# Optimization experiments

Hardware: AMD Instinct MI355X
Metric: run time of the kernel (lower is better)

The kernel has to match this reference:

```python
import jax, jax.numpy as jnp
import numpy as np

N, D_IN, D, C, TOPK = 8192, 1024, 512, 2, 6
SCALE = D ** -0.5
LN_EPS = 1e-5


def setup_inputs() -> dict:
    key = jax.random.key(0)
    ks = jax.random.split(key, 20)
    s = 0.02
    p = {
        'x': jax.random.normal(ks[0], (N, D_IN), jnp.float32),
        'fc1_w': jax.random.normal(ks[1], (D_IN, D)) * s,
        'fc1_b': jnp.zeros((D,)),
        'wh_w': jax.random.normal(ks[2], (D, D)) * s,
        'wh_b': jnp.zeros((D,)),
        'wt_w': jax.random.normal(ks[3], (D, D)) * s,
        'wt_b': jnp.zeros((D,)),
        'lin1_w': jax.random.normal(ks[4], (D, D)) * s,
        'lin1_b': jnp.zeros((D,)),
        'lin2_w': jax.random.normal(ks[5], (D, D)) * s,
        'lin2_b': jnp.zeros((D,)),
        'att1_w': jax.random.normal(ks[6], (D, D // 2)) * s,
        'att1_b': jnp.zeros((D // 2,)),
        'att2_w': jax.random.normal(ks[7], (D // 2, 1)) * s,
        'att2_b': jnp.zeros((1,)),
        'ln_g': jnp.ones((D,)),
        'ln_b': jnp.zeros((D,)),
        'fc_w': jax.random.normal(ks[8], (D, C)) * s,
        'fc_b': jnp.zeros((C,)),
    }
    return p


def reference(x, fc1_w, fc1_b, wh_w, wh_b, wt_w, wt_b, lin1_w, lin1_b,
              lin2_w, lin2_b, att1_w, att1_b, att2_w, att2_b, ln_g, ln_b,
              fc_w, fc_b):
    # _fc1: Linear + ReLU (dropout = eval identity)
    h = jax.nn.relu(x @ fc1_w + fc1_b)                      # [N, D]
    h = (h + h.mean(axis=0, keepdims=True)) * 0.5
    e_h = h @ wh_w + wh_b                                   # [N, D]
    e_t = h @ wt_w + wt_b                                   # [N, D]
    # dense N x N attention logits, then top-k neighbors
    logits = (e_h * SCALE) @ e_t.T                          # [N, N]
    tw, ti = jax.lax.top_k(logits, TOPK)                    # [N, K]
    Nb_h = e_t[ti]                                          # [N, K, D] gather
    p = jax.nn.softmax(tw, axis=-1)                         # [N, K]
    # eh_r = p * Nb_h + (1 - p) * e_h  (the matmul in torch is a broadcast)
    eh_r = p[..., None] * Nb_h + (1.0 - p)[..., None] * e_h[:, None, :]
    gate = jnp.tanh(e_h[:, None, :] + eh_r)                 # [N, K, D]
    ka = jnp.einsum('nkd,nkd->nk', Nb_h, gate)              # [N, K]
    kp = jax.nn.softmax(ka, axis=-1)                        # [N, K]
    e_Nh = jnp.einsum('nk,nkd->nd', kp, Nb_h)               # [N, D]
    sum_e = jax.nn.leaky_relu((e_h + e_Nh) @ lin1_w + lin1_b)
    bi_e = jax.nn.leaky_relu((e_h * e_Nh) @ lin2_w + lin2_b)
    emb = sum_e + bi_e                                      # [N, D]
    # GlobalAttention readout over all N nodes (batch=None -> one graph)
    att = jax.nn.leaky_relu(emb @ att1_w + att1_b) @ att2_w + att2_b  # [N,1]
    a = jax.nn.softmax(att, axis=0)                         # [N, 1]
    pooled = jnp.sum(a * emb, axis=0, keepdims=True)        # [1, D]
    # LayerNorm
    mu = pooled.mean(axis=-1, keepdims=True)
    var = pooled.var(axis=-1, keepdims=True)
    ln = (pooled - mu) * jax.lax.rsqrt(var + LN_EPS) * ln_g + ln_b
    out = ln @ fc_w + fc_b                                  # [1, C]
    Y_prob = jax.nn.softmax(out, axis=-1)
    Y_hat = jnp.argmax(out, axis=-1, keepdims=True)
    return out, Y_prob, Y_hat
```

## Files before the change

### kernel.cpp

```cpp
#include <hip/hip_runtime.h>
#include <hip/hip_bf16.h>
#include <cstdint>
#include <math.h>

typedef unsigned short u16;
typedef unsigned int u32;
typedef __bf16 bh;
typedef bh bh8 __attribute__((ext_vector_type(8)));
typedef float f32x4 __attribute__((ext_vector_type(4)));

#define SCALE_F 0.04419417382415922f

__device__ __forceinline__ float bf2f(u16 u) {
    union { float f; unsigned int i; } v; v.i = ((unsigned int)u) << 16; return v.f;
}
__device__ __forceinline__ u16 f2bf(float f) {
    __hip_bfloat16 h = __float2bfloat16(f);
    return __builtin_bit_cast(u16, h);
}
__device__ __forceinline__ bh8 ld8_f32(const float* p) {
    float4 f0 = *(const float4*)p;
    float4 f1 = *(const float4*)(p + 4);
    bh8 r;
    r[0] = (bh)f0.x; r[1] = (bh)f0.y; r[2] = (bh)f0.z; r[3] = (bh)f0.w;
    r[4] = (bh)f1.x; r[5] = (bh)f1.y; r[6] = (bh)f1.z; r[7] = (bh)f1.w;
    return r;
}

__device__ __forceinline__ u32 ordf(float f) {
    u32 u = __float_as_uint(f);
    return u ^ ((u32)((int)u >> 31) | 0x80000000u);
}
__device__ __forceinline__ float unordf(u32 s) {
    u32 u = (s & 0x80000000u) ? (s ^ 0x80000000u) : ~s;
    return __uint_as_float(u);
}
__device__ __forceinline__ u32 pack_vi(float v, int inv_idx) {
    return (ordf(v) & 0xFFFFFF00u) | (u32)inv_idx;
}
__device__ __forceinline__ float unpack_v(u32 p) {
    return unordf(p & 0xFFFFFF00u);
}

__device__ __forceinline__ void gl_lds16(const u16* g, u16* l) {
    __builtin_amdgcn_global_load_lds(
        (const __attribute__((address_space(1))) void*)g,
        (__attribute__((address_space(3))) void*)l, 16, 0, 0);
}

__global__ void transpose_cvt(const float* s0, u16* d0, const float* s1, u16* d1,
                              const float* s2, u16* d2, const float* s3, u16* d3,
                              const float* s4, u16* d4, const float* s5, u16* d5,
                              const float* xs, u16* xd) {
    int b = blockIdx.x;
    if (b >= 1664) {
        int t = threadIdx.y * 32 + threadIdx.x;
        size_t i = ((size_t)(b - 1664) * 256 + t) * 8;
        *(bh8*)(xd + i) = ld8_f32(xs + i);
        return;
    }
    __shared__ float tsh[32][33];
    const float* src; u16* dst; int R, C, tt;
    if      (b < 512)  { src = s0; dst = d0; R = 1024; C = 512; tt = b; }
    else if (b < 768)  { src = s1; dst = d1; R = 512;  C = 512; tt = b - 512; }
    else if (b < 1024) { src = s2; dst = d2; R = 512;  C = 512; tt = b - 768; }
    else if (b < 1280) { src = s3; dst = d3; R = 512;  C = 512; tt = b - 1024; }
    else if (b < 1536) { src = s4; dst = d4; R = 512;  C = 512; tt = b - 1280; }
    else               { src = s5; dst = d5; R = 512;  C = 256; tt = b - 1536; }
    int ntx = C >> 5;
    int bx = (tt % ntx) * 32, by = (tt / ntx) * 32;
    int x = threadIdx.x, y = threadIdx.y;
    for (int i = 0; i < 32; i += 8)
        tsh[y + i][x] = src[(size_t)(by + y + i) * C + bx + x];
    __syncthreads();
    for (int i = 0; i < 32; i += 8)
        dst[(size_t)(bx + y + i) * R + by + x] = f2bf(tsh[x][y + i]);
}

template<int KT, int NF>
__device__ __forceinline__ void kloop64(const u16* __restrict__ Ag, const u16* __restrict__ Bg,
                                        u16* Alds, u16* Blds, f32x4 (&acc)[2][NF]) {
    const int tid = threadIdx.x;
    const int wave = tid >> 6, lane = tid & 63;
    const int lr = lane & 15, quad = lane >> 4;
    const int wm = (wave & 1) * 32, wn = (wave >> 1) * (NF * 16);
    const int r = tid >> 2;
    const int g8 = (((tid & 3) ^ ((tid >> 3) & 3))) * 8;
    const int kbr8 = (quad ^ ((lr >> 1) & 3)) * 8;
    const u16* ga  = Ag + (size_t)r * KT + g8;
    const u16* gb0 = Bg + (size_t)r * KT + g8;
    const u16* gb1 = gb0 + (size_t)64 * KT;
    u16* la = Alds + wave * 512;
    u16* lb = Blds + wave * 512;
    #pragma unroll
    for (int k0 = 0; k0 < KT; k0 += 32) {
        __syncthreads();
        gl_lds16(ga + k0, la);
        gl_lds16(gb0 + k0, lb);
        if (NF == 4) gl_lds16(gb1 + k0, lb + 2048);
        __syncthreads();
        bh8 af[2], bf_[NF];
        #pragma unroll
        for (int i = 0; i < 2; i++)
            af[i] = *(const bh8*)&Alds[(wm + i * 16 + lr) * 32 + kbr8];
        #pragma unroll
        for (int i = 0; i < NF; i++)
            bf_[i] = *(const bh8*)&Blds[(wn + i * 16 + lr) * 32 + kbr8];
        #pragma unroll
        for (int mi = 0; mi < 2; mi++)
            #pragma unroll
            for (int ni = 0; ni < NF; ni++)
                acc[mi][ni] = __builtin_amdgcn_mfma_f32_16x16x32_bf16(
                    af[mi], bf_[ni], acc[mi][ni], 0, 0, 0);
    }
}

template<int ACT, int F32OUT>
__device__ __forceinline__ void epilogue64(f32x4 (&acc)[2][2], const float* bias,
                                           float* Cf, u16* Cb, int N, int m0, int n0) {
    const int tid = threadIdx.x;
    const int wave = tid >> 6, lane = tid & 63;
    const int lr = lane & 15, quad = lane >> 4;
    const int wm = (wave & 1) * 32, wn = (wave >> 1) * 32;
    #pragma unroll
    for (int ni = 0; ni < 2; ni++) {
        int col = n0 + wn + ni * 16 + lr;
        float bs = bias[col];
        #pragma unroll
        for (int mi = 0; mi < 2; mi++) {
            #pragma unroll
            for (int i = 0; i < 4; i++) {
                int row = m0 + wm + mi * 16 + quad * 4 + i;
                float v = acc[mi][ni][i] + bs;
                if (ACT == 1) v = fmaxf(v, 0.0f);
                if (ACT == 2) v = (v > 0.0f) ? v : 0.01f * v;
                size_t o = (size_t)row * N + col;
                if (F32OUT) Cf[o] = v;
                else        Cb[o] = f2bf(v);
            }
        }
    }
}

template<int ACT, int F32OUT, int KT>
__global__ __launch_bounds__(256) void gemm64(
    const u16* __restrict__ A, const u16* __restrict__ B, const float* __restrict__ bias,
    float* __restrict__ Cf, u16* __restrict__ Cb, int N)
{
    __shared__ __align__(16) u16 Alds[64 * 32];
    __shared__ __align__(16) u16 Blds[64 * 32];
    const int m0 = blockIdx.y * 64, n0 = blockIdx.x * 64;
    f32x4 acc[2][2] = {};
    kloop64<KT, 2>(A + (size_t)m0 * KT, B + (size_t)n0 * KT, Alds, Blds, acc);
    epilogue64<ACT, F32OUT>(acc, bias, Cf, Cb, N, m0, n0);
}

__global__ __launch_bounds__(256) void ehet64(
    const u16* __restrict__ A, const u16* __restrict__ Bh, const u16* __restrict__ Bt,
    const float* __restrict__ bh_, const float* __restrict__ bt_,
    u16* __restrict__ Oh, u16* __restrict__ Ot)
{
    __shared__ __align__(16) u16 Alds[64 * 32];
    __shared__ __align__(16) u16 Blds[64 * 32];
    const int bx = blockIdx.x;
    const int m0 = blockIdx.y * 64, n0 = (bx & 7) * 64;
    const u16* B = (bx < 8) ? Bh : Bt;
    const float* bias = (bx < 8) ? bh_ : bt_;
    u16* O = (bx < 8) ? Oh : Ot;
    f32x4 acc[2][2] = {};
    kloop64<512, 2>(A + (size_t)m0 * 512, B + (size_t)n0 * 512, Alds, Blds, acc);
    epilogue64<0, 0>(acc, bias, nullptr, O, 512, m0, n0);
}

__global__ __launch_bounds__(256) void lin12_64(
    const u16* __restrict__ A1, const u16* __restrict__ B1, const float* __restrict__ b1,
    const u16* __restrict__ A2, const u16* __restrict__ B2, const float* __restrict__ b2,
    u16* __restrict__ O)
{
    __shared__ __align__(16) u16 Alds[64 * 32];
    __shared__ __align__(16) u16 Blds[64 * 32];
    const int m0 = blockIdx.y * 64, n0 = blockIdx.x * 64;
    f32x4 acc1[2][2] = {}, acc2[2][2] = {};
    kloop64<512, 2>(A1 + (size_t)m0 * 512, B1 + (size_t)n0 * 512, Alds, Blds, acc1);
    kloop64<512, 2>(A2 + (size_t)m0 * 512, B2 + (size_t)n0 * 512, Alds, Blds, acc2);
    const int tid = threadIdx.x;
    const int wave = tid >> 6, lane = tid & 63;
    const int lr = lane & 15, quad = lane >> 4;
    const int wm = (wave & 1) * 32, wn = (wave >> 1) * 32;
    #pragma unroll
    for (int ni = 0; ni < 2; ni++) {
        int col = n0 + wn + ni * 16 + lr;
        float bs1 = b1[col], bs2 = b2[col];
        #pragma unroll
        for (int mi = 0; mi < 2; mi++) {
            #pragma unroll
            for (int i = 0; i < 4; i++) {
                int row = m0 + wm + mi * 16 + quad * 4 + i;
                float v1 = acc1[mi][ni][i] + bs1;
                v1 = (v1 > 0.0f) ? v1 : 0.01f * v1;
                float v2 = acc2[mi][ni][i] + bs2;
                v2 = (v2 > 0.0f) ? v2 : 0.01f * v2;
                O[(size_t)row * 512 + col] = f2bf(v1 + v2);
            }
        }
    }
}

__global__ __launch_bounds__(256) void logits_topk(
    const u16* __restrict__ Ah, const u16* __restrict__ Bt, u32* __restrict__ tvp)
{
    __shared__ __align__(16) u16 Alds[64 * 32];
    __shared__ __align__(16) u16 Blds[128 * 32];
    __shared__ u32 S[64 * 65];
    const int tid = threadIdx.x;
    const int m0 = blockIdx.y * 64;
    const int cb0 = blockIdx.x * 256;
    const int lane = tid & 63, wave = tid >> 6;
    const int wm = (wave & 1) * 32, wn = (wave >> 1) * 64;
    const int lr = lane & 15, quad = lane >> 4;
    const int srow = tid >> 2, scg = tid & 3;

    u32 v0 = 0, v1 = 0, v2 = 0, v3 = 0, v4 = 0, v5 = 0;

    for (int nt = 0; nt < 2; nt++) {
        f32x4 acc[2][4] = {};
        kloop64<512, 4>(Ah + (size_t)m0 * 512,
                        Bt + (size_t)(cb0 + nt * 128) * 512, Alds, Blds, acc);
        #pragma unroll
        for (int half = 0; half < 2; half++) {
            __syncthreads();
            if ((wave >> 1) == half) {
                #pragma unroll
                for (int mi = 0; mi < 2; mi++)
                    #pragma unroll
                    for (int ni = 0; ni < 4; ni++)
                        #pragma unroll
                        for (int i = 0; i < 4; i++) {
                            int colLocal = nt * 128 + half * 64 + ni * 16 + lr;
                            S[(wm + mi * 16 + quad * 4 + i) * 65 + ni * 16 + lr]
                                = pack_vi(acc[mi][ni][i], 255 - colLocal);
                        }
            }
            __syncthreads();
            const u32* Sr = &S[srow * 65 + scg * 16];
            #pragma unroll
            for (int c = 0; c < 16; c++) {
                u32 x = Sr[c];
                v5 = max(v5, min(v4, x));
                v4 = max(v4, min(v3, x));
                v3 = max(v3, min(v2, x));
                v2 = max(v2, min(v1, x));
                v1 = max(v1, min(v0, x));
                v0 = max(v0, x);
            }
        }
    }
    __syncthreads();
    {
        u32* dst = &S[srow * 65 + scg * 6];
        dst[0] = v0; dst[1] = v1; dst[2] = v2; dst[3] = v3; dst[4] = v4; dst[5] = v5;
    }
    __syncthreads();
    if (tid < 64) {
        u32 m0v = 0, m1v = 0, m2v = 0, m3v = 0, m4v = 0, m5v = 0;
        const u32* Sr = &S[tid * 65];
        #pragma unroll
        for (int s = 0; s < 24; s++) {
            u32 x = Sr[s];
            m5v = max(m5v, min(m4v, x));
            m4v = max(m4v, min(m3v, x));
            m3v = max(m3v, min(m2v, x));
            m2v = max(m2v, min(m1v, x));
            m1v = max(m1v, min(m0v, x));
            m0v = max(m0v, x);
        }
        u32* dst = tvp + (size_t)(m0 + tid) * 192 + blockIdx.x * 6;
        dst[0] = m0v; dst[1] = m1v; dst[2] = m2v;
        dst[3] = m3v; dst[4] = m4v; dst[5] = m5v;
    }
}

__global__ void topk_merge(const u32* __restrict__ tvp,
                           float* __restrict__ tv, int* __restrict__ ti)
{
    int r = blockIdx.x * 64 + threadIdx.x;
    u32 v[6]; int ix[6];
    #pragma unroll
    for (int j = 0; j < 6; j++) { v[j] = 0; ix[j] = 0; }
    const u32* pv = tvp + (size_t)r * 192;
    for (int b = 0; b < 32; b++) {
        #pragma unroll
        for (int j2 = 0; j2 < 6; j2++) {
            u32 p = pv[b * 6 + j2];
            if (p <= v[5]) break;
            v[5] = p; ix[5] = b * 256 + 255 - (int)(p & 255u);
            #pragma unroll
            for (int j = 5; j > 0; j--) {
                if (v[j] > v[j - 1]) {
                    u32 tf = v[j]; v[j] = v[j - 1]; v[j - 1] = tf;
                    int tx = ix[j]; ix[j] = ix[j - 1]; ix[j - 1] = tx;
                }
            }
        }
    }
    #pragma unroll
    for (int j = 0; j < 6; j++) {
        tv[(size_t)r * 6 + j] = unpack_v(v[j]) * SCALE_F;
        ti[(size_t)r * 6 + j] = ix[j];
    }
}

__global__ __launch_bounds__(256) void neighbor_kernel(
    const u16* __restrict__ eH, const u16* __restrict__ eT,
    const float* __restrict__ tv, const int* __restrict__ ti,
    u16* __restrict__ s1, u16* __restrict__ s2)
{
    const int tid = threadIdx.x, wave = tid >> 6, lane = tid & 63;
    const int n = blockIdx.x * 4 + wave;
    float tw[6]; int id[6];
    #pragma unroll
    for (int j = 0; j < 6; j++) {
        tw[j] = tv[n * 6 + j];
        int t = ti[n * 6 + j];
        id[j] = ((unsigned)t < 8192u) ? t : 0;
    }
    float mx = tw[0];
    #pragma unroll
    for (int j = 1; j < 6; j++) mx = fmaxf(mx, tw[j]);
    float p[6]; float ps = 0.f;
    #pragma unroll
    for (int j = 0; j < 6; j++) { p[j] = __expf(tw[j] - mx); ps += p[j]; }
    float inv = 1.0f / ps;
    #pragma unroll
    for (int j = 0; j < 6; j++) p[j] *= inv;

    const size_t base = (size_t)n * 512 + lane * 8;
    float eh[8];
    { bh8 v = *(const bh8*)(eH + base);
      #pragma unroll
      for (int c = 0; c < 8; c++) eh[c] = (float)v[c]; }
    float nb[6][8];
    #pragma unroll
    for (int j = 0; j < 6; j++) {
        bh8 v = *(const bh8*)(eT + (size_t)id[j] * 512 + lane * 8);
        #pragma unroll
        for (int c = 0; c < 8; c++) nb[j][c] = (float)v[c];
    }
    float ka[6];
    #pragma unroll
    for (int j = 0; j < 6; j++) {
        float s = 0.f;
        #pragma unroll
        for (int c = 0; c < 8; c++) {
            float e = p[j] * nb[j][c] + (1.f - p[j]) * eh[c];
            float x = eh[c] + e;
            x = fminf(fmaxf(x, -15.f), 15.f);
            float ex = __expf(2.f * x);
            float g = 1.f - 2.f / (ex + 1.f);
            s += nb[j][c] * g;
        }
        #pragma unroll
        for (int off = 32; off > 0; off >>= 1) s += __shfl_down(s, off);
        ka[j] = __shfl(s, 0);
    }
    float m2 = ka[0];
    #pragma unroll
    for (int j = 1; j < 6; j++) m2 = fmaxf(m2, ka[j]);
    float kp[6]; float ks = 0.f;
    #pragma unroll
    for (int j = 0; j < 6; j++) { kp[j] = __expf(ka[j] - m2); ks += kp[j]; }
    float inv2 = 1.0f / ks;
    #pragma unroll
    for (int j = 0; j < 6; j++) kp[j] *= inv2;
    bh8 o1, o2;
    #pragma unroll
    for (int c = 0; c < 8; c++) {
        float eN = 0.f;
        #pragma unroll
        for (int j = 0; j < 6; j++) eN += kp[j] * nb[j][c];
        o1[c] = (bh)(eh[c] + eN);
        o2[c] = (bh)(eh[c] * eN);
    }
    *(bh8*)(s1 + base) = o1;
    *(bh8*)(s2 + base) = o2;
}

__global__ void colsum_kernel(const u16* __restrict__ h, float* __restrict__ colsum) {
    int tid = threadIdx.x;
    int n0 = blockIdx.x * 32;
    float a0 = 0.f, a1 = 0.f;
    for (int k = 0; k < 32; k++) {
        size_t b = (size_t)(n0 + k) * 512;
        a0 += bf2f(h[b + tid]); a1 += bf2f(h[b + tid + 256]);
    }
    atomicAdd(&colsum[tid], a0);
    atomicAdd(&colsum[tid + 256], a1);
}

__global__ void meanmix_kernel(u16* __restrict__ h, const float* __restrict__ colsum) {
    size_t i = ((size_t)blockIdx.x * 256 + threadIdx.x) * 8;
    int col = (int)(i & 511);
    union { int4 v; u16 s[8]; } u;
    u.v = *(const int4*)&h[i];
    #pragma unroll
    for (int j = 0; j < 8; j++)
        u.s[j] = f2bf((bf2f(u.s[j]) + colsum[col + j] * (1.0f / 8192.0f)) * 0.5f);
    *(int4*)&h[i] = u.v;
}

__global__ __launch_bounds__(256) void att2_kernel(
    const float* __restrict__ a1, const float* __restrict__ w,
    const float* __restrict__ b, float* __restrict__ att)
{
    int row = blockIdx.x * 4 + (threadIdx.x >> 6);
    int lane = threadIdx.x & 63;
    const float* pr = a1 + (size_t)row * 256;
    float s = 0.f;
    #pragma unroll
    for (int k = 0; k < 4; k++) { int c = lane + k * 64; s += pr[c] * w[c]; }
    #pragma unroll
    for (int off = 32; off > 0; off >>= 1) s += __shfl_down(s, off);
    if (lane == 0) att[row] = s + b[0];
}

__global__ void att_max(const float* __restrict__ att, u32* __restrict__ scal_u) {
    int i = blockIdx.x * 256 + threadIdx.x;
    int lane = threadIdx.x & 63;
    u32 o = ordf(att[i]);
    #pragma unroll
    for (int off = 32; off > 0; off >>= 1) o = max(o, (u32)__shfl_down((int)o, off));
    if (lane == 0) atomicMax(&scal_u[0], o);
}
__global__ void att_sum(const float* __restrict__ att, float* __restrict__ scal) {
    int i = blockIdx.x * 256 + threadIdx.x;
    int lane = threadIdx.x & 63;
    float mx = unordf(((const u32*)scal)[0]);
    float e = __expf(att[i] - mx);
    #pragma unroll
    for (int off = 32; off > 0; off >>= 1) e += __shfl_down(e, off);
    if (lane == 0) atomicAdd(&scal[1], e);
}

__global__ void pooled_kernel(const u16* __restrict__ emb, const float* __restrict__ att,
                              const float* __restrict__ scal, float* __restrict__ pooled) {
    int tid = threadIdx.x;
    int n0 = blockIdx.x * 32;
    float mx = unordf(((const u32*)scal)[0]);
    float inv = 1.0f / scal[1];
    float a0 = 0.f, a1 = 0.f;
    for (int k = 0; k < 32; k++) {
        int n = n0 + k;
        float w = __expf(att[n] - mx) * inv;
        size_t b = (size_t)n * 512;
        a0 += w * bf2f(emb[b + tid]);
        a1 += w * bf2f(emb[b + tid + 256]);
    }
    atomicAdd(&pooled[tid], a0);
    atomicAdd(&pooled[tid + 256], a1);
}

__global__ void final_kernel(const float* __restrict__ pooled,
                             const float* __restrict__ g, const float* __restrict__ bln,
                             const float* __restrict__ fcw, const float* __restrict__ fcb,
                             float* __restrict__ out) {
    __shared__ float red[256];
    int tid = threadIdx.x;
    float x0 = pooled[tid], x1 = pooled[tid + 256];
    red[tid] = x0 + x1; __syncthreads();
    for (int s = 128; s > 0; s >>= 1) { if (tid < s) red[tid] += red[tid + s]; __syncthreads(); }
    float mu = red[0] * (1.0f / 512.0f); __syncthreads();
    float d0 = x0 - mu, d1 = x1 - mu;
    red[tid] = d0 * d0 + d1 * d1; __syncthreads();
    for (int s = 128; s > 0; s >>= 1) { if (tid < s) red[tid] += red[tid + s]; __syncthreads(); }
    float var = red[0] * (1.0f / 512.0f); __syncthreads();
    float rstd = rsqrtf(var + 1e-5f);
    float l0 = d0 * rstd * g[tid]       + bln[tid];
    float l1 = d1 * rstd * g[tid + 256] + bln[tid + 256];
    red[tid] = l0 * fcw[tid * 2] + l1 * fcw[(tid + 256) * 2]; __syncthreads();
    for (int s = 128; s > 0; s >>= 1) { if (tid < s) red[tid] += red[tid + s]; __syncthreads(); }
    float o0 = red[0] + fcb[0]; __syncthreads();
    red[tid] = l0 * fcw[tid * 2 + 1] + l1 * fcw[(tid + 256) * 2 + 1]; __syncthreads();
    for (int s = 128; s > 0; s >>= 1) { if (tid < s) red[tid] += red[tid + s]; __syncthreads(); }
    float o1 = red[0] + fcb[1];
    if (tid == 0) {
        float m = fmaxf(o0, o1);
        float e0 = expf(o0 - m), e1 = expf(o1 - m);
        float se = e0 + e1;
        out[0] = o0;
        out[1] = o1;
        out[2] = e0 / se;
        out[3] = e1 / se;
        out[4] = (o0 >= o1) ? 0.0f : 1.0f;
    }
}

extern "C" void kernel_launch(void* const* d_in, const int* in_sizes, int n_in,
                              void* d_out, int out_size, void* d_ws, size_t ws_size,
                              hipStream_t stream)
{
    const float* x      = (const float*)d_in[0];
    const float* fc1_w  = (const float*)d_in[1];
    const float* fc1_b  = (const float*)d_in[2];
    const float* wh_w   = (const float*)d_in[3];
    const float* wh_b   = (const float*)d_in[4];
    const float* wt_w   = (const float*)d_in[5];
    const float* wt_b   = (const float*)d_in[6];
    const float* lin1_w = (const float*)d_in[7];
    const float* lin1_b = (const float*)d_in[8];
    const float* lin2_w = (const float*)d_in[9];
    const float* lin2_b = (const float*)d_in[10];
    const float* att1_w = (const float*)d_in[11];
    const float* att1_b = (const float*)d_in[12];
    const float* att2_w = (const float*)d_in[13];
    const float* att2_b = (const float*)d_in[14];
    const float* ln_g   = (const float*)d_in[15];
    const float* ln_b   = (const float*)d_in[16];
    const float* fc_w   = (const float*)d_in[17];
    const float* fc_b   = (const float*)d_in[18];
    float* out = (float*)d_out;
    char* ws = (char*)d_ws;

    u16*   fc1T   = (u16*)(ws + 0);
    u16*   whT    = (u16*)(ws + 1048576);
    u16*   wtT    = (u16*)(ws + 1572864);
    u16*   l1T    = (u16*)(ws + 2097152);
    u16*   l2T    = (u16*)(ws + 2621440);
    u16*   a1T    = (u16*)(ws + 3145728);
    float* tv     = (float*)(ws + 3407872);
    int*   ti     = (int*)(ws + 3604480);
    float* att    = (float*)(ws + 3801088);
    float* colsum = (float*)(ws + 3833856);
    float* pooled = (float*)(ws + 3835904);
    float* scal   = (float*)(ws + 3837952);
    u32*   tvp    = (u32*)(ws + 4194304);
    u16*   hbf    = (u16*)(ws + 14680064);
    u16*   ehbf   = (u16*)(ws + 23068672);
    u16*   etbf   = (u16*)(ws + 31457280);
    u16*   s2bf   = (u16*)(ws + 39845888);
    u16*   xbf    = (u16*)(ws + 23068672);
    float* a1f    = (float*)(ws + 23068672);

    transpose_cvt<<<5760, dim3(32, 8), 0, stream>>>(
        fc1_w, fc1T, wh_w, whT, wt_w, wtT, lin1_w, l1T, lin2_w, l2T, att1_w, a1T, x, xbf);
    hipMemsetAsync(colsum, 0, 4160, stream);

    gemm64<1, 0, 1024><<<dim3(8, 128), 256, 0, stream>>>(xbf, fc1T, fc1_b, nullptr, hbf, 512);
    colsum_kernel<<<256, 256, 0, stream>>>(hbf, colsum);
    meanmix_kernel<<<2048, 256, 0, stream>>>(hbf, colsum);

    ehet64<<<dim3(16, 128), 256, 0, stream>>>(hbf, whT, wtT, wh_b, wt_b, ehbf, etbf);

    logits_topk<<<dim3(32, 128), 256, 0, stream>>>(ehbf, etbf, tvp);
    topk_merge<<<128, 64, 0, stream>>>(tvp, tv, ti);

    neighbor_kernel<<<2048, 256, 0, stream>>>(ehbf, etbf, tv, ti, hbf, s2bf);

    lin12_64<<<dim3(8, 128), 256, 0, stream>>>(hbf, l1T, lin1_b, s2bf, l2T, lin2_b, etbf);

    gemm64<2, 1, 512><<<dim3(4, 128), 256, 0, stream>>>(etbf, a1T, att1_b, a1f, nullptr, 256);
    att2_kernel<<<2048, 256, 0, stream>>>(a1f, att2_w, att2_b, att);
    att_max<<<32, 256, 0, stream>>>(att, (u32*)scal);
    att_sum<<<32, 256, 0, stream>>>(att, scal);
    pooled_kernel<<<256, 256, 0, stream>>>(etbf, att, scal, pooled);

    final_kernel<<<1, 256, 0, stream>>>(pooled, ln_g, ln_b, fc_w, fc_b, out);
}
```

Baseline: 381.2 us.

## Widen logits_topk to 512 threads and fuse att1 GEMM with att2 reduction

The logits_topk kernel now runs 512 threads per block and computes all 256 columns of a block tile in one K loop. A and two B tiles are loaded straight into LDS with swizzled addressing, and the top-6 scan uses vector LDS reads over 8-element chunks. Separately, the att1 GEMM epilogue applies bias, leaky ReLU and the att2 dot product in registers, then reduces into att with atomics. This removes the fp32 a1 intermediate and the att2 kernel. The changes add atomic contention and a widened memset, and the larger block may lower occupancy.

Result: no change. 382.9 us (+0.4%).

```diff
diff --git a/kernel.cpp b/kernel.cpp
--- a/kernel.cpp
+++ b/kernel.cpp
@@ -47,6 +47,11 @@
         (const __attribute__((address_space(1))) void*)g,
         (__attribute__((address_space(3))) void*)l, 16, 0, 0);
 }
+
+#define TOP6_INS(x) do { u32 _x = (x); \
+    v5 = max(v5, min(v4, _x)); v4 = max(v4, min(v3, _x)); \
+    v3 = max(v3, min(v2, _x)); v2 = max(v2, min(v1, _x)); \
+    v1 = max(v1, min(v0, _x)); v0 = max(v0, _x); } while (0)
 
 __global__ void transpose_cvt(const float* s0, u16* d0, const float* s1, u16* d1,
                               const float* s2, u16* d2, const float* s3, u16* d3,
@@ -206,66 +211,126 @@
     }
 }
 
-__global__ __launch_bounds__(256) void logits_topk(
+__global__ __launch_bounds__(256) void att1_fused(
+    const u16* __restrict__ A, const u16* __restrict__ B, const float* __restrict__ bias,
+    const float* __restrict__ w2, const float* __restrict__ b2, float* __restrict__ att)
+{
+    __shared__ __align__(16) u16 Alds[64 * 32];
+    __shared__ __align__(16) u16 Blds[64 * 32];
+    const int m0 = blockIdx.y * 64, n0 = blockIdx.x * 64;
+    f32x4 acc[2][2] = {};
+    kloop64<512, 2>(A + (size_t)m0 * 512, B + (size_t)n0 * 512, Alds, Blds, acc);
+    const int tid = threadIdx.x;
+    const int wave = tid >> 6, lane = tid & 63;
+    const int lr = lane & 15, quad = lane >> 4;
+    const int wm = (wave & 1) * 32, wn = (wave >> 1) * 32;
+    float rp[2][4] = {};
+    #pragma unroll
+    for (int ni = 0; ni < 2; ni++) {
+        int col = n0 + wn + ni * 16 + lr;
+        float bs = bias[col], wv = w2[col];
+        #pragma unroll
+        for (int mi = 0; mi < 2; mi++)
+            #pragma unroll
+            for (int i = 0; i < 4; i++) {
+                float v = acc[mi][ni][i] + bs;
+                v = (v > 0.0f) ? v : 0.01f * v;
+                rp[mi][i] += v * wv;
+            }
+    }
+    float badd = (blockIdx.x == 0 && wn == 0) ? b2[0] : 0.0f;
+    #pragma unroll
+    for (int mi = 0; mi < 2; mi++)
+        #pragma unroll
+        for (int i = 0; i < 4; i++) {
+            float s = rp[mi][i];
+            s += __shfl_xor(s, 1); s += __shfl_xor(s, 2);
+            s += __shfl_xor(s, 4); s += __shfl_xor(s, 8);
+            if (lr == 0)
+                atomicAdd(&att[m0 + wm + mi * 16 + quad * 4 + i], s + badd);
+        }
+}
+
+__global__ __launch_bounds__(512) void logits_topk(
     const u16* __restrict__ Ah, const u16* __restrict__ Bt, u32* __restrict__ tvp)
 {
     __shared__ __align__(16) u16 Alds[64 * 32];
-    __shared__ __align__(16) u16 Blds[128 * 32];
-    __shared__ u32 S[64 * 65];
+    __shared__ __align__(16) u16 Blds[256 * 32];
+    __shared__ __align__(16) u32 S[64 * 68];
     const int tid = threadIdx.x;
     const int m0 = blockIdx.y * 64;
     const int cb0 = blockIdx.x * 256;
     const int lane = tid & 63, wave = tid >> 6;
     const int wm = (wave & 1) * 32, wn = (wave >> 1) * 64;
     const int lr = lane & 15, quad = lane >> 4;
-    const int srow = tid >> 2, scg = tid & 3;
+    const int kbr8 = (quad ^ ((lr >> 1) & 3)) * 8;
+    const int g8 = (((tid & 3) ^ ((tid >> 3) & 3))) * 8;
+    const int r = tid >> 2;
+    const u16* gA  = Ah + (size_t)(m0 + r) * 512 + g8;
+    const u16* gB0 = Bt + (size_t)(cb0 + r) * 512 + g8;
+    const u16* gB1 = Bt + (size_t)(cb0 + 128 + r) * 512 + g8;
+    u16* la  = Alds + wave * 512;
+    u16* lb0 = Blds + wave * 512;
+    u16* lb1 = Blds + wave * 512 + 4096;
+
+    f32x4 acc[2][4] = {};
+    #pragma unroll
+    for (int k0 = 0; k0 < 512; k0 += 32) {
+        __syncthreads();
+        if (tid < 256) gl_lds16(gA + k0, la);
+        gl_lds16(gB0 + k0, lb0);
+        gl_lds16(gB1 + k0, lb1);
+        __syncthreads();
+        bh8 af[2], bf_[4];
+        #pragma unroll
+        for (int i = 0; i < 2; i++)
+            af[i] = *(const bh8*)&Alds[(wm + i * 16 + lr) * 32 + kbr8];
+        #pragma unroll
+        for (int i = 0; i < 4; i++)
+            bf_[i] = *(const bh8*)&Blds[(wn + i * 16 + lr) * 32 + kbr8];
+        #pragma unroll
+        for (int mi = 0; mi < 2; mi++)
+            #pragma unroll
+            for (int ni = 0; ni < 4; ni++)
+                acc[mi][ni] = __builtin_amdgcn_mfma_f32_16x16x32_bf16(
+                    af[mi], bf_[ni], acc[mi][ni], 0, 0, 0);
+    }
 
     u32 v0 = 0, v1 = 0, v2 = 0, v3 = 0, v4 = 0, v5 = 0;
-
-    for (int nt = 0; nt < 2; nt++) {
-        f32x4 acc[2][4] = {};
-        kloop64<512, 4>(Ah + (size_t)m0 * 512,
-                        Bt + (size_t)(cb0 + nt * 128) * 512, Alds, Blds, acc);
-        #pragma unroll
-        for (int half = 0; half < 2; half++) {
-            __syncthreads();
-            if ((wave >> 1) == half) {
+    const int srow = tid >> 3, scg = tid & 7;
+    #pragma unroll
+    for (int half = 0; half < 4; half++) {
+        __syncthreads();
+        if ((wave >> 1) == half) {
+            #pragma unroll
+            for (int mi = 0; mi < 2; mi++)
                 #pragma unroll
-                for (int mi = 0; mi < 2; mi++)
+                for (int ni = 0; ni < 4; ni++)
                     #pragma unroll
-                    for (int ni = 0; ni < 4; ni++)
-                        #pragma unroll
-                        for (int i = 0; i < 4; i++) {
-                            int colLocal = nt * 128 + half * 64 + ni * 16 + lr;
-                            S[(wm + mi * 16 + quad * 4 + i) * 65 + ni * 16 + lr]
-                                = pack_vi(acc[mi][ni][i], 255 - colLocal);
-                        }
-            }
-            __syncthreads();
-            const u32* Sr = &S[srow * 65 + scg * 16];
-            #pragma unroll
-            for (int c = 0; c < 16; c++) {
-                u32 x = Sr[c];
-                v5 = max(v5, min(v4, x));
-                v4 = max(v4, min(v3, x));
-                v3 = max(v3, min(v2, x));
-                v2 = max(v2, min(v1, x));
-                v1 = max(v1, min(v0, x));
-                v0 = max(v0, x);
-            }
+                    for (int i = 0; i < 4; i++) {
+                        int colLocal = wn + ni * 16 + lr;
+                        S[(wm + mi * 16 + quad * 4 + i) * 68 + ni * 16 + lr]
+                            = pack_vi(acc[mi][ni][i], 255 - colLocal);
+                    }
         }
+        __syncthreads();
+        const u32* Sr = &S[srow * 68 + scg * 8];
+        uint4 a = *(const uint4*)Sr;
+        uint4 b = *(const uint4*)(Sr + 4);
+        TOP6_INS(a.x); TOP6_INS(a.y); TOP6_INS(a.z); TOP6_INS(a.w);
+        TOP6_INS(b.x); TOP6_INS(b.y); TOP6_INS(b.z); TOP6_INS(b.w);
     }
     __syncthreads();
     {
-        u32* dst = &S[srow * 65 + scg * 6];
+        u32* dst = &S[srow * 68 + scg * 6];
         dst[0] = v0; dst[1] = v1; dst[2] = v2; dst[3] = v3; dst[4] = v4; dst[5] = v5;
     }
     __syncthreads();
     if (tid < 64) {
         u32 m0v = 0, m1v = 0, m2v = 0, m3v = 0, m4v = 0, m5v = 0;
-        const u32* Sr = &S[tid * 65];
-        #pragma unroll
-        for (int s = 0; s < 24; s++) {
+        const u32* Sr = &S[tid * 68];
+        #pragma unroll
+        for (int s = 0; s < 48; s++) {
             u32 x = Sr[s];
             m5v = max(m5v, min(m4v, x));
             m4v = max(m4v, min(m3v, x));
@@ -406,21 +471,6 @@
     for (int j = 0; j < 8; j++)
         u.s[j] = f2bf((bf2f(u.s[j]) + colsum[col + j] * (1.0f / 8192.0f)) * 0.5f);
     *(int4*)&h[i] = u.v;
-}
-
-__global__ __launch_bounds__(256) void att2_kernel(
-    const float* __restrict__ a1, const float* __restrict__ w,
-    const float* __restrict__ b, float* __restrict__ att)
-{
-    int row = blockIdx.x * 4 + (threadIdx.x >> 6);
-    int lane = threadIdx.x & 63;
-    const float* pr = a1 + (size_t)row * 256;
-    float s = 0.f;
-    #pragma unroll
-    for (int k = 0; k < 4; k++) { int c = lane + k * 64; s += pr[c] * w[c]; }
-    #pragma unroll
-    for (int off = 32; off > 0; off >>= 1) s += __shfl_down(s, off);
-    if (lane == 0) att[row] = s + b[0];
 }
 
 __global__ void att_max(const float* __restrict__ att, u32* __restrict__ scal_u) {
@@ -538,11 +588,10 @@
     u16*   etbf   = (u16*)(ws + 31457280);
     u16*   s2bf   = (u16*)(ws + 39845888);
     u16*   xbf    = (u16*)(ws + 23068672);
-    float* a1f    = (float*)(ws + 23068672);
 
     transpose_cvt<<<5760, dim3(32, 8), 0, stream>>>(
         fc1_w, fc1T, wh_w, whT, wt_w, wtT, lin1_w, l1T, lin2_w, l2T, att1_w, a1T, x, xbf);
-    hipMemsetAsync(colsum, 0, 4160, stream);
+    hipMemsetAsync(att, 0, 36928, stream);
 
     gemm64<1, 0, 1024><<<dim3(8, 128), 256, 0, stream>>>(xbf, fc1T, fc1_b, nullptr, hbf, 512);
     colsum_kernel<<<256, 256, 0, stream>>>(hbf, colsum);
@@ -550,15 +599,14 @@
 
     ehet64<<<dim3(16, 128), 256, 0, stream>>>(hbf, whT, wtT, wh_b, wt_b, ehbf, etbf);
 
-    logits_topk<<<dim3(32, 128), 256, 0, stream>>>(ehbf, etbf, tvp);
+    logits_topk<<<dim3(32, 128), 512, 0, stream>>>(ehbf, etbf, tvp);
     topk_merge<<<128, 64, 0, stream>>>(tvp, tv, ti);
 
     neighbor_kernel<<<2048, 256, 0, stream>>>(ehbf, etbf, tv, ti, hbf, s2bf);
 
     lin12_64<<<dim3(8, 128), 256, 0, stream>>>(hbf, l1T, lin1_b, s2bf, l2T, lin2_b, etbf);
 
-    gemm64<2, 1, 512><<<dim3(4, 128), 256, 0, stream>>>(etbf, a1T, att1_b, a1f, nullptr, 256);
-    att2_kernel<<<2048, 256, 0, stream>>>(a1f, att2_w, att2_b, att);
+    att1_fused<<<dim3(4, 128), 256, 0, stream>>>(etbf, a1T, att1_b, att2_w, att2_b, att);
     att_max<<<32, 256, 0, stream>>>(att, (u32*)scal);
     att_sum<<<32, 256, 0, stream>>>(att, scal);
     pooled_kernel<<<256, 256, 0, stream>>>(etbf, att, scal, pooled);
```
